# Kernel tuning notes

Hardware: AMD Instinct MI355X
Metric: run time of the kernel (lower is better)

## Reference

```python
import jax, jax.numpy as jnp
import numpy as np

B, T, S, I, H = 64, 64, 512, 512, 512

def setup_inputs() -> dict:
    key = jax.random.key(0)
    ks = jax.random.split(key, 9)
    sc = 0.02
    return {
        "input": jax.random.normal(ks[0], (B, T, I), jnp.float32),
        "h0": jax.random.normal(ks[1], (B, H), jnp.float32),
        "c0": jax.random.normal(ks[2], (B, H), jnp.float32),
        "ctx": jax.random.normal(ks[3], (S, B, H), jnp.float32),
        "W_ih": jax.random.normal(ks[4], (4 * H, I), jnp.float32) * sc,
        "b_ih": jax.random.normal(ks[5], (4 * H,), jnp.float32) * sc,
        "W_hh": jax.random.normal(ks[6], (4 * H, H), jnp.float32) * sc,
        "b_hh": jax.random.normal(ks[7], (4 * H,), jnp.float32) * sc,
        "W_out": jax.random.normal(ks[8], (H, 2 * H), jnp.float32) * sc,
    }

def reference(input, h0, c0, ctx, W_ih, b_ih, W_hh, b_hh, W_out):
    ctx_b = ctx.transpose(1, 0, 2)          # (B, S, H)
    x_tm = input.transpose(1, 0, 2)          # (T, B, I) time-major

    def step(carry, x):
        hx, cx = carry
        gates = x @ W_ih.T + b_ih + hx @ W_hh.T + b_hh   # (B, 4H)
        i, f, g, o = jnp.split(gates, 4, axis=1)          # chunk order: in, forget, cell, out
        ct = jax.nn.sigmoid(f) * cx + jax.nn.sigmoid(i) * jnp.tanh(g)
        ht = jax.nn.sigmoid(o) * jnp.tanh(ct)
        # dot attention over source positions
        scores = jnp.einsum('bsh,bh->bs', ctx_b, ht)      # (B, S)
        attn = jax.nn.softmax(scores, axis=1)
        wc = jnp.einsum('bs,bsh->bh', attn, ctx_b)        # (B, H)
        h_tilde = jnp.tanh(jnp.concatenate([wc, ht], axis=1) @ W_out.T)
        return (ht, ct), h_tilde

    (hT, cT), out = jax.lax.scan(step, (h0, c0), x_tm)    # out: (T, B, H)
    return out.transpose(1, 0, 2), hT, cT
```

## Files before the change

kernel.cpp:

```cpp
#include <hip/hip_runtime.h>
#include <hip/hip_bf16.h>

#define NB 64
#define NT_ 64
#define NS 512
#define NI 512
#define NH 512
#define G4 2048
#define H2 1024
#define BT (NB*NT_)
#define RBLK 64
#define CPB 8

typedef __attribute__((ext_vector_type(8))) short short8;
typedef __attribute__((ext_vector_type(4))) float f32x4;

__device__ __forceinline__ short f2bs(float f) {
    __hip_bfloat16 h = __float2bfloat16(f);
    return *reinterpret_cast<short*>(&h);
}
__device__ __forceinline__ float bs2f(short s) {
    unsigned int u = ((unsigned int)(unsigned short)s) << 16;
    union { unsigned int u; float f; } c; c.u = u; return c.f;
}
__device__ __forceinline__ short8 ld8b(const __hip_bfloat16* p) {
    return *reinterpret_cast<const short8*>(p);
}
__device__ __forceinline__ void ld8f2(const float* p, short8& hi, short8& lo) {
    float4 a = *reinterpret_cast<const float4*>(p);
    float4 b = *reinterpret_cast<const float4*>(p + 4);
    float v[8] = {a.x,a.y,a.z,a.w,b.x,b.y,b.z,b.w};
    #pragma unroll
    for (int i = 0; i < 8; i++) {
        short h = f2bs(v[i]);
        hi[i] = h;
        lo[i] = f2bs(v[i] - bs2f(h));
    }
}
__device__ __forceinline__ float fsigm(float x){ return 1.f/(1.f + __expf(-x)); }
__device__ __forceinline__ float ftanh(float x){ float e = __expf(2.f*x); return 1.f - 2.f/(e + 1.f); }

__global__ __launch_bounds__(256) void conv_split(const float* __restrict__ s,
                                                  __hip_bfloat16* __restrict__ hi,
                                                  __hip_bfloat16* __restrict__ lo, int n) {
    for (int i = blockIdx.x*256 + threadIdx.x; i < n; i += gridDim.x*256) {
        float x = s[i];
        __hip_bfloat16 h = __float2bfloat16(x);
        hi[i] = h;
        lo[i] = __float2bfloat16(x - __bfloat162float(h));
    }
}

__global__ __launch_bounds__(256) void hseq0_init(const float* __restrict__ h0,
                                                  __hip_bfloat16* __restrict__ hs_h,
                                                  __hip_bfloat16* __restrict__ hs_l,
                                                  unsigned* __restrict__ flags) {
    int i = blockIdx.x*256 + threadIdx.x;
    if (i < RBLK*32) flags[i] = 0u;
    if (i < NB*NH) {
        float x = h0[i];
        __hip_bfloat16 h = __float2bfloat16(x);
        hs_h[i] = h;
        hs_l[i] = __float2bfloat16(x - __bfloat162float(h));
    }
}

__global__ __launch_bounds__(256) void transpose_ctx(const float* __restrict__ ctx,
                                                     __hip_bfloat16* __restrict__ ctxT) {
    __shared__ float tile[64][65];
    int s0 = blockIdx.x*64, h0 = blockIdx.y*64, b = blockIdx.z;
    int tx = threadIdx.x & 63, ty = threadIdx.x >> 6;
    for (int i = 0; i < 16; i++) {
        int s = i*4 + ty;
        tile[s][tx] = ctx[(size_t)(s0+s)*NB*NH + (size_t)b*NH + h0 + tx];
    }
    __syncthreads();
    for (int i = 0; i < 16; i++) {
        int h = i*4 + ty;
        ctxT[(size_t)b*NH*NS + (size_t)(h0+h)*NS + s0 + tx] = __float2bfloat16(tile[tx][h]);
    }
}

__global__ __launch_bounds__(256) void gemm_xw(const float* __restrict__ X,
                                               const __hip_bfloat16* __restrict__ Wh,
                                               const __hip_bfloat16* __restrict__ Wl,
                                               const float* __restrict__ b_ih,
                                               const float* __restrict__ b_hh,
                                               float* __restrict__ XW) {
    int wid = blockIdx.x*4 + (threadIdx.x>>6);
    int lane = threadIdx.x & 63;
    int m0 = (wid >> 5) * 64;
    int n0 = (wid & 31) * 64;
    int fr = lane & 15, fq = lane >> 4;
    f32x4 acc[4][4] = {};
    for (int kk = 0; kk < NI; kk += 32) {
        short8 ah[4], al[4], bh[4], bl[4];
        #pragma unroll
        for (int i = 0; i < 4; i++) ld8f2(X + (size_t)(m0+i*16+fr)*NI + kk + fq*8, ah[i], al[i]);
        #pragma unroll
        for (int j = 0; j < 4; j++) {
            bh[j] = ld8b(Wh + (size_t)(n0+j*16+fr)*NI + kk + fq*8);
            bl[j] = ld8b(Wl + (size_t)(n0+j*16+fr)*NI + kk + fq*8);
        }
        #pragma unroll
        for (int i = 0; i < 4; i++)
            #pragma unroll
            for (int j = 0; j < 4; j++) {
                acc[i][j] = __builtin_amdgcn_mfma_f32_16x16x32_bf16(ah[i], bh[j], acc[i][j], 0,0,0);
                acc[i][j] = __builtin_amdgcn_mfma_f32_16x16x32_bf16(ah[i], bl[j], acc[i][j], 0,0,0);
                acc[i][j] = __builtin_amdgcn_mfma_f32_16x16x32_bf16(al[i], bh[j], acc[i][j], 0,0,0);
            }
    }
    #pragma unroll
    for (int i = 0; i < 4; i++)
      #pragma unroll
      for (int j = 0; j < 4; j++)
        #pragma unroll
        for (int r = 0; r < 4; r++) {
            int m = m0 + i*16 + fq*4 + r;
            int n = n0 + j*16 + fr;
            XW[(size_t)m*G4 + n] = acc[i][j][r] + b_ih[n] + b_hh[n];
        }
}

__global__ __launch_bounds__(256, 1) void lstm_persist(
    const float* __restrict__ c0,
    const __hip_bfloat16* __restrict__ Whh_h,
    const __hip_bfloat16* __restrict__ Whh_l,
    const float* __restrict__ XW,
    __hip_bfloat16* __restrict__ hs_h,
    __hip_bfloat16* __restrict__ hs_l,
    float* __restrict__ hT, float* __restrict__ cT,
    unsigned* __restrict__ flags)
{
    __shared__ __hip_bfloat16 Wh[32*512];
    __shared__ __hip_bfloat16 Wl[32*512];
    __shared__ float gl[4][32][33];
    int tid = threadIdx.x, bi = blockIdx.x;
    int lane = tid & 63, w = tid >> 6;
    int fr = lane & 15, fq = lane >> 4;

    {
        int jl = tid >> 3, ck8 = tid & 7;
        int grow = (jl >> 3) * NH + bi * CPB + (jl & 7);
        const short8* srcH = (const short8*)(Whh_h + (size_t)grow * NH);
        const short8* srcL = (const short8*)(Whh_l + (size_t)grow * NH);
        #pragma unroll
        for (int cc = 0; cc < 8; cc++) {
            int ck = ck8 * 8 + cc;
            int sw = (ck * 16) ^ ((jl & 7) << 4);
            *(short8*)((char*)Wh + jl * 1024 + sw) = srcH[ck];
            *(short8*)((char*)Wl + jl * 1024 + sw) = srcL[ck];
        }
    }
    int eb  = tid >> 2;
    int ec0 = (tid & 3) * 2;
    int ebl = eb & 31, mhalf = eb >> 5;
    float creg[2];
    creg[0] = c0[eb * NH + bi*CPB + ec0];
    creg[1] = c0[eb * NH + bi*CPB + ec0 + 1];
    float xw[8];
    #pragma unroll
    for (int g = 0; g < 4; g++)
      #pragma unroll
      for (int u = 0; u < 2; u++)
        xw[g*2+u] = XW[(size_t)eb*NT_*G4 + g*NH + bi*CPB + ec0 + u];
    __syncthreads();

    int m0 = (w & 1) * 32;
    int kbase = (w >> 1) * 256;

    for (int t = 0; t < NT_; t++) {
        const __hip_bfloat16* Ah = hs_h + (size_t)t * NB * NH;
        const __hip_bfloat16* Al = hs_l + (size_t)t * NB * NH;

        f32x4 acc[2][2] = {};
        #pragma unroll
        for (int kk = 0; kk < 256; kk += 32) {
            short8 a_h[2], a_l[2], b_h[2], b_l[2];
            #pragma unroll
            for (int i = 0; i < 2; i++) {
                size_t off = (size_t)(m0 + i*16 + fr) * NH + kbase + kk + fq*8;
                a_h[i] = ld8b(Ah + off);
                a_l[i] = ld8b(Al + off);
            }
            #pragma unroll
            for (int j = 0; j < 2; j++) {
                int jl = j*16 + fr;
                int byt = jl*1024 + ((((kbase + kk + fq*8)*2)) ^ ((jl & 7) << 4));
                b_h[j] = *(const short8*)((const char*)Wh + byt);
                b_l[j] = *(const short8*)((const char*)Wl + byt);
            }
            #pragma unroll
            for (int i = 0; i < 2; i++)
                #pragma unroll
                for (int j = 0; j < 2; j++) {
                    acc[i][j] = __builtin_amdgcn_mfma_f32_16x16x32_bf16(a_h[i], b_h[j], acc[i][j], 0,0,0);
                    acc[i][j] = __builtin_amdgcn_mfma_f32_16x16x32_bf16(a_h[i], b_l[j], acc[i][j], 0,0,0);
                    acc[i][j] = __builtin_amdgcn_mfma_f32_16x16x32_bf16(a_l[i], b_h[j], acc[i][j], 0,0,0);
                }
        }
        #pragma unroll
        for (int i = 0; i < 2; i++)
          #pragma unroll
          for (int j = 0; j < 2; j++)
            #pragma unroll
            for (int r = 0; r < 4; r++)
                gl[w][i*16 + fq*4 + r][j*16 + fr] = acc[i][j][r];
        __syncthreads();

        float hv[2];
        #pragma unroll
        for (int u = 0; u < 2; u++) {
            int cl = ec0 + u;
            float gi = gl[mhalf][ebl][cl]      + gl[2+mhalf][ebl][cl]      + xw[u];
            float gf = gl[mhalf][ebl][8 + cl]  + gl[2+mhalf][ebl][8 + cl]  + xw[2+u];
            float gg = gl[mhalf][ebl][16 + cl] + gl[2+mhalf][ebl][16 + cl] + xw[4+u];
            float go = gl[mhalf][ebl][24 + cl] + gl[2+mhalf][ebl][24 + cl] + xw[6+u];
            float ct = fsigm(gf)*creg[u] + fsigm(gi)*ftanh(gg);
            hv[u] = fsigm(go)*ftanh(ct);
            creg[u] = ct;
        }
        int hcol = bi*CPB + ec0;
        size_t hoff = (size_t)(t+1)*NB*NH + (size_t)eb*NH + hcol;
        unsigned short h0b = (unsigned short)f2bs(hv[0]);
        unsigned short h1b = (unsigned short)f2bs(hv[1]);
        unsigned ph = (unsigned)h0b | ((unsigned)h1b << 16);
        unsigned short l0b = (unsigned short)f2bs(hv[0] - bs2f((short)h0b));
        unsigned short l1b = (unsigned short)f2bs(hv[1] - bs2f((short)h1b));
        unsigned pl = (unsigned)l0b | ((unsigned)l1b << 16);
        __hip_atomic_store((unsigned*)&hs_h[hoff], ph, __ATOMIC_RELAXED, __HIP_MEMORY_SCOPE_AGENT);
        __hip_atomic_store((unsigned*)&hs_l[hoff], pl, __ATOMIC_RELAXED, __HIP_MEMORY_SCOPE_AGENT);
        if (t == NT_-1) {
            *(float2*)&hT[(size_t)eb*NH + hcol] = make_float2(hv[0], hv[1]);
            *(float2*)&cT[(size_t)eb*NH + hcol] = make_float2(creg[0], creg[1]);
        }

        asm volatile("s_waitcnt vmcnt(0)" ::: "memory");
        __syncthreads();
        if (tid == 0)
            __hip_atomic_store(&flags[bi*32], (unsigned)(t+1), __ATOMIC_RELAXED, __HIP_MEMORY_SCOPE_AGENT);
        if (t + 1 < NT_) {
            #pragma unroll
            for (int g = 0; g < 4; g++)
              #pragma unroll
              for (int u = 0; u < 2; u++)
                xw[g*2+u] = XW[((size_t)eb*NT_ + (t+1))*G4 + g*NH + bi*CPB + ec0 + u];
        }
        if (w == 0) {
            unsigned target = (unsigned)(t+1);
            int guard = 0;
            while (__hip_atomic_load(&flags[lane*32], __ATOMIC_RELAXED, __HIP_MEMORY_SCOPE_AGENT) < target) {
                __builtin_amdgcn_s_sleep(1);
                if (++guard > (1<<22)) break;
            }
        }
        __syncthreads();
    }
}

__global__ __launch_bounds__(256) void gemm_scores(const __hip_bfloat16* __restrict__ hs_h,
                                                   const __hip_bfloat16* __restrict__ hs_l,
                                                   const float* __restrict__ ctx,
                                                   float* __restrict__ scores) {
    int wid = blockIdx.x*4 + (threadIdx.x>>6);
    int lane = threadIdx.x & 63;
    int b  = wid >> 3;
    int n0 = (wid & 7) * 64;
    int fr = lane & 15, fq = lane >> 4;
    const __hip_bfloat16* Abh = hs_h + NB*NH + (size_t)b*NH;
    const __hip_bfloat16* Abl = hs_l + NB*NH + (size_t)b*NH;
    const float* Bb = ctx + (size_t)b*NH;
    f32x4 acc[4][4] = {};
    for (int kk = 0; kk < NH; kk += 32) {
        short8 ah[4], al[4], bh[4], bl[4];
        #pragma unroll
        for (int i = 0; i < 4; i++) {
            size_t off = (size_t)(i*16+fr)*NB*NH + kk + fq*8;
            ah[i] = ld8b(Abh + off);
            al[i] = ld8b(Abl + off);
        }
        #pragma unroll
        for (int j = 0; j < 4; j++) ld8f2(Bb + (size_t)(n0+j*16+fr)*NB*NH + kk + fq*8, bh[j], bl[j]);
        #pragma unroll
        for (int i = 0; i < 4; i++)
            #pragma unroll
            for (int j = 0; j < 4; j++) {
                acc[i][j] = __builtin_amdgcn_mfma_f32_16x16x32_bf16(ah[i], bh[j], acc[i][j], 0,0,0);
                acc[i][j] = __builtin_amdgcn_mfma_f32_16x16x32_bf16(ah[i], bl[j], acc[i][j], 0,0,0);
                acc[i][j] = __builtin_amdgcn_mfma_f32_16x16x32_bf16(al[i], bh[j], acc[i][j], 0,0,0);
            }
    }
    #pragma unroll
    for (int i = 0; i < 4; i++)
      #pragma unroll
      for (int j = 0; j < 4; j++)
        #pragma unroll
        for (int r = 0; r < 4; r++) {
            int t = i*16 + fq*4 + r;
            int s = n0 + j*16 + fr;
            scores[((size_t)b*NT_ + t)*NS + s] = acc[i][j][r];
        }
}

__global__ __launch_bounds__(256) void softmax_rows(const float* __restrict__ scores,
                                                    __hip_bfloat16* __restrict__ ah,
                                                    __hip_bfloat16* __restrict__ al) {
    int row = blockIdx.x*4 + (threadIdx.x>>6);
    int lane = threadIdx.x & 63;
    const float* r = scores + (size_t)row*NS;
    float v[8], mx = -1e30f;
    #pragma unroll
    for (int i = 0; i < 8; i++) { v[i] = r[lane + i*64]; mx = fmaxf(mx, v[i]); }
    #pragma unroll
    for (int off = 32; off; off >>= 1) mx = fmaxf(mx, __shfl_xor(mx, off));
    float sum = 0.f;
    #pragma unroll
    for (int i = 0; i < 8; i++) { v[i] = __expf(v[i]-mx); sum += v[i]; }
    #pragma unroll
    for (int off = 32; off; off >>= 1) sum += __shfl_xor(sum, off);
    float inv = 1.f/sum;
    #pragma unroll
    for (int i = 0; i < 8; i++) {
        float a = v[i]*inv;
        __hip_bfloat16 h = __float2bfloat16(a);
        ah[(size_t)row*NS + lane + i*64] = h;
        al[(size_t)row*NS + lane + i*64] = __float2bfloat16(a - __bfloat162float(h));
    }
}

__global__ __launch_bounds__(256) void gemm_wc(const __hip_bfloat16* __restrict__ Ah,
                                               const __hip_bfloat16* __restrict__ Al,
                                               const __hip_bfloat16* __restrict__ ctxT,
                                               float* __restrict__ Wc) {
    int wid = blockIdx.x*4 + (threadIdx.x>>6);
    int lane = threadIdx.x & 63;
    int b  = wid >> 3;
    int n0 = (wid & 7) * 64;
    int fr = lane & 15, fq = lane >> 4;
    const __hip_bfloat16* Abh = Ah + (size_t)b*NT_*NS;
    const __hip_bfloat16* Abl = Al + (size_t)b*NT_*NS;
    const __hip_bfloat16* Bb  = ctxT + (size_t)b*NH*NS;
    f32x4 acc[4][4] = {};
    for (int kk = 0; kk < NS; kk += 32) {
        short8 ah[4], al[4], bb[4];
        #pragma unroll
        for (int i = 0; i < 4; i++) {
            ah[i] = ld8b(Abh + (size_t)(i*16+fr)*NS + kk + fq*8);
            al[i] = ld8b(Abl + (size_t)(i*16+fr)*NS + kk + fq*8);
        }
        #pragma unroll
        for (int j = 0; j < 4; j++) bb[j] = ld8b(Bb + (size_t)(n0+j*16+fr)*NS + kk + fq*8);
        #pragma unroll
        for (int i = 0; i < 4; i++)
            #pragma unroll
            for (int j = 0; j < 4; j++) {
                acc[i][j] = __builtin_amdgcn_mfma_f32_16x16x32_bf16(ah[i], bb[j], acc[i][j], 0,0,0);
                acc[i][j] = __builtin_amdgcn_mfma_f32_16x16x32_bf16(al[i], bb[j], acc[i][j], 0,0,0);
            }
    }
    #pragma unroll
    for (int i = 0; i < 4; i++)
      #pragma unroll
      for (int j = 0; j < 4; j++)
        #pragma unroll
        for (int r = 0; r < 4; r++) {
            int t = i*16 + fq*4 + r;
            int h = n0 + j*16 + fr;
            Wc[((size_t)b*NT_ + t)*NH + h] = acc[i][j][r];
        }
}

__global__ __launch_bounds__(256) void gemm_out(const float* __restrict__ Wc,
                                                const __hip_bfloat16* __restrict__ hs_h,
                                                const __hip_bfloat16* __restrict__ hs_l,
                                                const __hip_bfloat16* __restrict__ Wh,
                                                const __hip_bfloat16* __restrict__ Wl,
                                                float* __restrict__ out) {
    int wid = blockIdx.x*4 + (threadIdx.x>>6);
    int lane = threadIdx.x & 63;
    int m0 = (wid >> 3) * 64;
    int n0 = (wid & 7) * 64;
    int fr = lane & 15, fq = lane >> 4;
    f32x4 acc[4][4] = {};
    for (int kk = 0; kk < NH; kk += 32) {
        short8 ah[4], al[4], bh[4], bl[4];
        #pragma unroll
        for (int i = 0; i < 4; i++) ld8f2(Wc + (size_t)(m0+i*16+fr)*NH + kk + fq*8, ah[i], al[i]);
        #pragma unroll
        for (int j = 0; j < 4; j++) {
            bh[j] = ld8b(Wh + (size_t)(n0+j*16+fr)*H2 + kk + fq*8);
            bl[j] = ld8b(Wl + (size_t)(n0+j*16+fr)*H2 + kk + fq*8);
        }
        #pragma unroll
        for (int i = 0; i < 4; i++)
            #pragma unroll
            for (int j = 0; j < 4; j++) {
                acc[i][j] = __builtin_amdgcn_mfma_f32_16x16x32_bf16(ah[i], bh[j], acc[i][j], 0,0,0);
                acc[i][j] = __builtin_amdgcn_mfma_f32_16x16x32_bf16(ah[i], bl[j], acc[i][j], 0,0,0);
                acc[i][j] = __builtin_amdgcn_mfma_f32_16x16x32_bf16(al[i], bh[j], acc[i][j], 0,0,0);
            }
    }
    {
        const __hip_bfloat16* A2h = hs_h + NB*NH + (size_t)(m0>>6)*NH;
        const __hip_bfloat16* A2l = hs_l + NB*NH + (size_t)(m0>>6)*NH;
        for (int kk = 0; kk < NH; kk += 32) {
            short8 ah[4], al[4], bh[4], bl[4];
            #pragma unroll
            for (int i = 0; i < 4; i++) {
                size_t off = (size_t)(i*16+fr)*NB*NH + kk + fq*8;
                ah[i] = ld8b(A2h + off);
                al[i] = ld8b(A2l + off);
            }
            #pragma unroll
            for (int j = 0; j < 4; j++) {
                bh[j] = ld8b(Wh + (size_t)(n0+j*16+fr)*H2 + NH + kk + fq*8);
                bl[j] = ld8b(Wl + (size_t)(n0+j*16+fr)*H2 + NH + kk + fq*8);
            }
            #pragma unroll
            for (int i = 0; i < 4; i++)
                #pragma unroll
                for (int j = 0; j < 4; j++) {
                    acc[i][j] = __builtin_amdgcn_mfma_f32_16x16x32_bf16(ah[i], bh[j], acc[i][j], 0,0,0);
                    acc[i][j] = __builtin_amdgcn_mfma_f32_16x16x32_bf16(ah[i], bl[j], acc[i][j], 0,0,0);
                    acc[i][j] = __builtin_amdgcn_mfma_f32_16x16x32_bf16(al[i], bh[j], acc[i][j], 0,0,0);
                }
        }
    }
    #pragma unroll
    for (int i = 0; i < 4; i++)
      #pragma unroll
      for (int j = 0; j < 4; j++)
        #pragma unroll
        for (int r = 0; r < 4; r++) {
            int m = m0 + i*16 + fq*4 + r;
            int n = n0 + j*16 + fr;
            out[(size_t)m*NH + n] = ftanh(acc[i][j][r]);
        }
}


extern "C" void kernel_launch(void* const* d_in, const int* in_sizes, int n_in,
                              void* d_out, int out_size, void* d_ws, size_t ws_size,
                              hipStream_t stream) {
    const float* input = (const float*)d_in[0];
    const float* h0    = (const float*)d_in[1];
    const float* c0    = (const float*)d_in[2];
    const float* ctx   = (const float*)d_in[3];
    const float* W_ih  = (const float*)d_in[4];
    const float* b_ih  = (const float*)d_in[5];
    const float* W_hh  = (const float*)d_in[6];
    const float* b_hh  = (const float*)d_in[7];
    const float* W_out = (const float*)d_in[8];
    float* out = (float*)d_out;

    const size_t OFF_XW     = 0;
    const size_t OFF_SCORES = 0;
    const size_t OFF_ATTN_H = 8388608;
    const size_t OFF_ATTN_L = 12582912;
    const size_t OFF_HS_H   = 33554432;
    const size_t OFF_HS_L   = 37814272;
    const size_t OFF_FLAGS  = 42074112;
    const size_t OFF_WC     = 42082304;
    const size_t OFF_WIH_H  = 50470912;
    const size_t OFF_WIH_L  = 52568064;
    const size_t OFF_WHH_H  = 54665216;
    const size_t OFF_WHH_L  = 56762368;
    const size_t OFF_WOUT_H = 58859520;
    const size_t OFF_WOUT_L = 59908096;
    const size_t OFF_CTXT   = 60956672;
    if (ws_size < 94511104u) return;

    char* ws = (char*)d_ws;
    float*          XW     = (float*)(ws + OFF_XW);
    float*          scores = (float*)(ws + OFF_SCORES);
    __hip_bfloat16* attn_h = (__hip_bfloat16*)(ws + OFF_ATTN_H);
    __hip_bfloat16* attn_l = (__hip_bfloat16*)(ws + OFF_ATTN_L);
    __hip_bfloat16* hs_h   = (__hip_bfloat16*)(ws + OFF_HS_H);
    __hip_bfloat16* hs_l   = (__hip_bfloat16*)(ws + OFF_HS_L);
    unsigned*       flags  = (unsigned*)(ws + OFF_FLAGS);
    float*          Wc     = (float*)(ws + OFF_WC);
    __hip_bfloat16* Wih_h  = (__hip_bfloat16*)(ws + OFF_WIH_H);
    __hip_bfloat16* Wih_l  = (__hip_bfloat16*)(ws + OFF_WIH_L);
    __hip_bfloat16* Whh_h  = (__hip_bfloat16*)(ws + OFF_WHH_H);
    __hip_bfloat16* Whh_l  = (__hip_bfloat16*)(ws + OFF_WHH_L);
    __hip_bfloat16* Wout_h = (__hip_bfloat16*)(ws + OFF_WOUT_H);
    __hip_bfloat16* Wout_l = (__hip_bfloat16*)(ws + OFF_WOUT_L);
    __hip_bfloat16* ctxT   = (__hip_bfloat16*)(ws + OFF_CTXT);

    conv_split<<<2048, 256, 0, stream>>>(W_ih, Wih_h, Wih_l, G4*NI);
    conv_split<<<2048, 256, 0, stream>>>(W_hh, Whh_h, Whh_l, G4*NH);
    conv_split<<<1024, 256, 0, stream>>>(W_out, Wout_h, Wout_l, NH*H2);
    hseq0_init<<<128, 256, 0, stream>>>(h0, hs_h, hs_l, flags);
    gemm_xw<<<512, 256, 0, stream>>>(input, Wih_h, Wih_l, b_ih, b_hh, XW);

    float* hT = out + (size_t)BT*NH;
    float* cT = hT + NB*NH;
    lstm_persist<<<RBLK, 256, 0, stream>>>(c0, Whh_h, Whh_l, XW, hs_h, hs_l, hT, cT, flags);

    transpose_ctx<<<dim3(8,8,64), 256, 0, stream>>>(ctx, ctxT);
    gemm_scores<<<128, 256, 0, stream>>>(hs_h, hs_l, ctx, scores);
    softmax_rows<<<1024, 256, 0, stream>>>(scores, attn_h, attn_l);
    gemm_wc<<<128, 256, 0, stream>>>(attn_h, attn_l, ctxT, Wc);
    gemm_out<<<128, 256, 0, stream>>>(Wc, hs_h, hs_l, Wout_h, Wout_l, out);
}
```

Measured before the change: 658.3 us.

## Pre-split input to bf16 pairs, hoist recurrent A loads, drop per-step barrier

Adds a conv_split pass that turns the input into hi/lo bf16 arrays so gemm_xw no longer splits the fp32 data inside its inner loop. In the persistent LSTM kernel, all A-operand (hidden state) fragments for a step are loaded into registers up front, before the MFMA loop, rather than being interleaved with it. Every wave now spins on the flags itself, which removes the trailing __syncthreads on each timestep. Risks include extra register pressure, more polling traffic, and an extra conversion pass whose buffers share workspace space with Wc.

Result: no change. 666.9 us (median of 2 runs) (+1.3%).

```diff
diff --git a/kernel.cpp b/kernel.cpp
--- a/kernel.cpp
+++ b/kernel.cpp
@@ -81,7 +81,8 @@
     }
 }
 
-__global__ __launch_bounds__(256) void gemm_xw(const float* __restrict__ X,
+__global__ __launch_bounds__(256) void gemm_xw(const __hip_bfloat16* __restrict__ Xh,
+                                               const __hip_bfloat16* __restrict__ Xl,
                                                const __hip_bfloat16* __restrict__ Wh,
                                                const __hip_bfloat16* __restrict__ Wl,
                                                const float* __restrict__ b_ih,
@@ -96,7 +97,11 @@
     for (int kk = 0; kk < NI; kk += 32) {
         short8 ah[4], al[4], bh[4], bl[4];
         #pragma unroll
-        for (int i = 0; i < 4; i++) ld8f2(X + (size_t)(m0+i*16+fr)*NI + kk + fq*8, ah[i], al[i]);
+        for (int i = 0; i < 4; i++) {
+            size_t off = (size_t)(m0+i*16+fr)*NI + kk + fq*8;
+            ah[i] = ld8b(Xh + off);
+            al[i] = ld8b(Xl + off);
+        }
         #pragma unroll
         for (int j = 0; j < 4; j++) {
             bh[j] = ld8b(Wh + (size_t)(n0+j*16+fr)*NI + kk + fq*8);
@@ -174,20 +179,26 @@
         const __hip_bfloat16* Ah = hs_h + (size_t)t * NB * NH;
         const __hip_bfloat16* Al = hs_l + (size_t)t * NB * NH;
 
+        short8 Aregh[2][8], Aregl[2][8];
+        #pragma unroll
+        for (int i = 0; i < 2; i++) {
+            const __hip_bfloat16* rowH = Ah + (size_t)(m0 + i*16 + fr) * NH + kbase + fq*8;
+            const __hip_bfloat16* rowL = Al + (size_t)(m0 + i*16 + fr) * NH + kbase + fq*8;
+            #pragma unroll
+            for (int k8 = 0; k8 < 8; k8++) {
+                Aregh[i][k8] = ld8b(rowH + k8*32);
+                Aregl[i][k8] = ld8b(rowL + k8*32);
+            }
+        }
+
         f32x4 acc[2][2] = {};
         #pragma unroll
-        for (int kk = 0; kk < 256; kk += 32) {
-            short8 a_h[2], a_l[2], b_h[2], b_l[2];
-            #pragma unroll
-            for (int i = 0; i < 2; i++) {
-                size_t off = (size_t)(m0 + i*16 + fr) * NH + kbase + kk + fq*8;
-                a_h[i] = ld8b(Ah + off);
-                a_l[i] = ld8b(Al + off);
-            }
+        for (int k8 = 0; k8 < 8; k8++) {
+            short8 b_h[2], b_l[2];
             #pragma unroll
             for (int j = 0; j < 2; j++) {
                 int jl = j*16 + fr;
-                int byt = jl*1024 + ((((kbase + kk + fq*8)*2)) ^ ((jl & 7) << 4));
+                int byt = jl*1024 + ((((kbase + k8*32 + fq*8)*2)) ^ ((jl & 7) << 4));
                 b_h[j] = *(const short8*)((const char*)Wh + byt);
                 b_l[j] = *(const short8*)((const char*)Wl + byt);
             }
@@ -195,9 +206,9 @@
             for (int i = 0; i < 2; i++)
                 #pragma unroll
                 for (int j = 0; j < 2; j++) {
-                    acc[i][j] = __builtin_amdgcn_mfma_f32_16x16x32_bf16(a_h[i], b_h[j], acc[i][j], 0,0,0);
-                    acc[i][j] = __builtin_amdgcn_mfma_f32_16x16x32_bf16(a_h[i], b_l[j], acc[i][j], 0,0,0);
-                    acc[i][j] = __builtin_amdgcn_mfma_f32_16x16x32_bf16(a_l[i], b_h[j], acc[i][j], 0,0,0);
+                    acc[i][j] = __builtin_amdgcn_mfma_f32_16x16x32_bf16(Aregh[i][k8], b_h[j], acc[i][j], 0,0,0);
+                    acc[i][j] = __builtin_amdgcn_mfma_f32_16x16x32_bf16(Aregh[i][k8], b_l[j], acc[i][j], 0,0,0);
+                    acc[i][j] = __builtin_amdgcn_mfma_f32_16x16x32_bf16(Aregl[i][k8], b_h[j], acc[i][j], 0,0,0);
                 }
         }
         #pragma unroll
@@ -247,7 +258,7 @@
               for (int u = 0; u < 2; u++)
                 xw[g*2+u] = XW[((size_t)eb*NT_ + (t+1))*G4 + g*NH + bi*CPB + ec0 + u];
         }
-        if (w == 0) {
+        {
             unsigned target = (unsigned)(t+1);
             int guard = 0;
             while (__hip_atomic_load(&flags[lane*32], __ATOMIC_RELAXED, __HIP_MEMORY_SCOPE_AGENT) < target) {
@@ -255,7 +266,6 @@
                 if (++guard > (1<<22)) break;
             }
         }
-        __syncthreads();
     }
 }
 
@@ -462,6 +472,8 @@
     const size_t OFF_HS_L   = 37814272;
     const size_t OFF_FLAGS  = 42074112;
     const size_t OFF_WC     = 42082304;
+    const size_t OFF_XH     = 42082304;
+    const size_t OFF_XL     = 46276608;
     const size_t OFF_WIH_H  = 50470912;
     const size_t OFF_WIH_L  = 52568064;
     const size_t OFF_WHH_H  = 54665216;
@@ -480,6 +492,8 @@
     __hip_bfloat16* hs_l   = (__hip_bfloat16*)(ws + OFF_HS_L);
     unsigned*       flags  = (unsigned*)(ws + OFF_FLAGS);
     float*          Wc     = (float*)(ws + OFF_WC);
+    __hip_bfloat16* Xh     = (__hip_bfloat16*)(ws + OFF_XH);
+    __hip_bfloat16* Xl     = (__hip_bfloat16*)(ws + OFF_XL);
     __hip_bfloat16* Wih_h  = (__hip_bfloat16*)(ws + OFF_WIH_H);
     __hip_bfloat16* Wih_l  = (__hip_bfloat16*)(ws + OFF_WIH_L);
     __hip_bfloat16* Whh_h  = (__hip_bfloat16*)(ws + OFF_WHH_H);
@@ -491,8 +505,9 @@
     conv_split<<<2048, 256, 0, stream>>>(W_ih, Wih_h, Wih_l, G4*NI);
     conv_split<<<2048, 256, 0, stream>>>(W_hh, Whh_h, Whh_l, G4*NH);
     conv_split<<<1024, 256, 0, stream>>>(W_out, Wout_h, Wout_l, NH*H2);
+    conv_split<<<2048, 256, 0, stream>>>(input, Xh, Xl, BT*NI);
     hseq0_init<<<128, 256, 0, stream>>>(h0, hs_h, hs_l, flags);
-    gemm_xw<<<512, 256, 0, stream>>>(input, Wih_h, Wih_l, b_ih, b_hh, XW);
+    gemm_xw<<<512, 256, 0, stream>>>(Xh, Xl, Wih_h, Wih_l, b_ih, b_hh, XW);
 
     float* hT = out + (size_t)BT*NH;
     float* cT = hT + NB*NH;
```
